# Kernel tuning notes

Measured on AMD Instinct MI355X. Metric: run time of the kernel, lower is better.

## Reference

```python
import math
import jax, jax.numpy as jnp
import numpy as np

D_MODEL = 1024
N_HEADS = 16
D_HEAD = D_MODEL // N_HEADS
MAX_REL = 1024
B = 2
S = 1024


def setup_inputs() -> dict:
    key = jax.random.key(0)
    ks = jax.random.split(key, 12)
    inp = {
        'query': jax.random.normal(ks[0], (B, S, D_MODEL), dtype=jnp.float32),
        'key': jax.random.normal(ks[1], (B, S, D_MODEL), dtype=jnp.float32),
        'value': jax.random.normal(ks[2], (B, S, D_MODEL), dtype=jnp.float32),
        # projection weights (torch nn.Linear: y = x @ W.T + b)
        'Wq': jax.random.normal(ks[3], (D_MODEL, D_MODEL), dtype=jnp.float32) / math.sqrt(D_MODEL),
        'bq': jax.random.normal(ks[4], (D_MODEL,), dtype=jnp.float32) * 0.02,
        'Wk': jax.random.normal(ks[5], (D_MODEL, D_MODEL), dtype=jnp.float32) / math.sqrt(D_MODEL),
        'bk': jax.random.normal(ks[6], (D_MODEL,), dtype=jnp.float32) * 0.02,
        'Wv': jax.random.normal(ks[7], (D_MODEL, D_MODEL), dtype=jnp.float32) / math.sqrt(D_MODEL),
        'bv': jax.random.normal(ks[8], (D_MODEL,), dtype=jnp.float32) * 0.02,
        # relative position tables (mask_future=True -> (max_rel, d_head))
        'rel_pos': jax.random.uniform(ks[9], (MAX_REL, D_HEAD), dtype=jnp.float32),
        'val_rel_pos': jax.random.uniform(ks[10], (MAX_REL, D_HEAD), dtype=jnp.float32),
    }
    return inp


def _rel_repr(table, seq_len):
    # mask_future=True branch: seq_len <= max_rel -> simple slice
    return table[:seq_len]  # [S, d_head]


def reference(query, key, value, Wq, bq, Wk, bk, Wv, bv, rel_pos, val_rel_pos):
    n_batch, seq_len, d_model = query.shape
    H, Dh = N_HEADS, D_HEAD

    def proj(x, W, b):
        return (x @ W.T + b).reshape(n_batch, seq_len, H, Dh).transpose(0, 2, 1, 3)

    q = proj(query, Wq, bq)   # [B,H,S,Dh]
    k = proj(key, Wk, bk)
    v = proj(value, Wv, bv)

    attn = jnp.einsum('bhid,bhjd->bhij', q, k)  # [B,H,S,S]

    # relative position bias via Music-Transformer skew trick (faithful to source)
    er = _rel_repr(rel_pos, seq_len)                 # [S, Dh]
    qe = jnp.einsum('bhid,rd->bhir', q, er)          # q @ er.T
    qe = jnp.flip(qe, axis=-1)
    qe = jnp.pad(qe, ((0, 0), (0, 0), (0, 0), (1, 0)))
    qe = qe.reshape(n_batch, H, seq_len + 1, seq_len)[:, :, 1:, :]
    attn = (attn + qe) / math.sqrt(Dh)               # source scales AFTER adding qe

    # causal future mask
    fmask = jnp.triu(jnp.ones((seq_len, seq_len), dtype=bool), k=1)
    attn = jnp.where(fmask[None, None], -jnp.inf, attn)
    attn = jax.nn.softmax(attn, axis=-1)

    z = jnp.einsum('bhij,bhjd->bhid', attn, v)

    # value relative position: zr[i] = sum_{j<=i} attn[i,j] * erv[i-j]
    # (equivalent to the source's flip/unfold construction of vr)
    erv = _rel_repr(val_rel_pos, seq_len)            # [S, Dh]
    i = jnp.arange(seq_len)[:, None]
    r = jnp.arange(seq_len)[None, :]
    j = i - r                                        # column index for relative dist r
    valid = (j >= 0).astype(attn.dtype)
    jc = jnp.clip(j, 0, seq_len - 1)
    attn_rel = jnp.take_along_axis(attn, jc[None, None], axis=-1) * valid[None, None]
    z = z + jnp.einsum('bhir,rd->bhid', attn_rel, erv)

    z = z.transpose(0, 2, 1, 3).reshape(n_batch, seq_len, d_model)
    return z
```

## Files before the change

kernel.cpp:

```cpp
#include <hip/hip_runtime.h>

typedef __bf16 bf16x8 __attribute__((ext_vector_type(8)));
typedef float f32x4 __attribute__((ext_vector_type(4)));

#define MFMA(a, b, c) __builtin_amdgcn_mfma_f32_16x16x32_bf16((a), (b), (c), 0, 0, 0)

#define DPPF(x, ctrl) __builtin_bit_cast(float, __builtin_amdgcn_mov_dpp(__builtin_bit_cast(int, (x)), (ctrl), 0xF, 0xF, true))

static __device__ __forceinline__ float rowmax16(float v) {
    v = fmaxf(v, DPPF(v, 0xB1));
    v = fmaxf(v, DPPF(v, 0x4E));
    v = fmaxf(v, DPPF(v, 0x124));
    v = fmaxf(v, DPPF(v, 0x128));
    return v;
}
static __device__ __forceinline__ float rowsum16(float v) {
    v += DPPF(v, 0xB1);
    v += DPPF(v, 0x4E);
    v += DPPF(v, 0x124);
    v += DPPF(v, 0x128);
    return v;
}

static __device__ __forceinline__ unsigned short f2b(float f) {
    unsigned int u = __builtin_bit_cast(unsigned int, f);
    unsigned int lsb = (u >> 16) & 1u;
    u += 0x7fffu + lsb;
    return (unsigned short)(u >> 16);
}

static __device__ __forceinline__ f32x4 zero4() {
    f32x4 z; z[0] = 0.f; z[1] = 0.f; z[2] = 0.f; z[3] = 0.f; return z;
}

typedef __attribute__((address_space(3))) unsigned int lds_as_t;
typedef const __attribute__((address_space(1))) unsigned int glb_as_t;
static __device__ __forceinline__ void gload16(const void* g, void* l) {
    __builtin_amdgcn_global_load_lds((glb_as_t*)g, (lds_as_t*)l, 16, 0, 0);
}

__global__ __launch_bounds__(256) void prep_convert(
    const float* __restrict__ q, const float* __restrict__ k, const float* __restrict__ v,
    const float* __restrict__ wq, const float* __restrict__ wk, const float* __restrict__ wv,
    const float* __restrict__ rel, const float* __restrict__ vrel,
    unsigned short* __restrict__ xq, unsigned short* __restrict__ xk, unsigned short* __restrict__ xv,
    unsigned short* __restrict__ wqb, unsigned short* __restrict__ wkb, unsigned short* __restrict__ wvb,
    unsigned short* __restrict__ erb, unsigned short* __restrict__ ervT)
{
    const int NG = 2375680;
    for (int g = blockIdx.x * 256 + threadIdx.x; g < NG + 69632; g += gridDim.x * 256) {
        if (g < NG) {
            const float* src; unsigned short* dst; int off;
            if (g < 1572864) {
                int s = g / 524288; off = g - s * 524288;
                src = s == 0 ? q : s == 1 ? k : v;
                dst = s == 0 ? xq : s == 1 ? xk : xv;
            } else if (g < 2359296) {
                int s = (g - 1572864) / 262144; off = g - 1572864 - s * 262144;
                src = s == 0 ? wq : s == 1 ? wk : wv;
                dst = s == 0 ? wqb : s == 1 ? wkb : wvb;
            } else {
                off = g - 2359296; src = rel; dst = erb;
            }
            float4 x = *(const float4*)(src + (size_t)off * 4);
            *(ushort4*)(dst + (size_t)off * 4) =
                make_ushort4(f2b(x.x), f2b(x.y), f2b(x.z), f2b(x.w));
        } else {
            int j = g - NG;
            int dh = j / 1088, c = j % 1088, r = c - 47;
            ervT[j] = (r >= 0 && r < 1024) ? f2b(vrel[r * 64 + dh]) : (unsigned short)0;
        }
    }
}

__global__ __launch_bounds__(256, 4) void proj_gemm2(
    const unsigned short* __restrict__ xq, const unsigned short* __restrict__ xk,
    const unsigned short* __restrict__ xv,
    const unsigned short* __restrict__ wqb, const unsigned short* __restrict__ wkb,
    const unsigned short* __restrict__ wvb,
    const float* __restrict__ bqp, const float* __restrict__ bkp, const float* __restrict__ bvp,
    unsigned short* __restrict__ oq, unsigned short* __restrict__ ok, unsigned short* __restrict__ ov)
{
    __shared__ unsigned short As[128][64];
    __shared__ unsigned short Bs[64][64];

    const int tid = threadIdx.x, lane = tid & 63, w = tid >> 6;
    const int bid = blockIdx.x;
    const int swz = (bid & 7) * 96 + (bid >> 3);
    const int mt = swz >> 4, nt = swz & 15;
    const int z = mt >> 4;
    const int mm0 = (mt & 15) * 128, n0 = nt * 64;

    const unsigned short* X = z == 0 ? xq : z == 1 ? xk : xv;
    const unsigned short* W = z == 0 ? wqb : z == 1 ? wkb : wvb;
    const float* bias = z == 0 ? bqp : z == 1 ? bkp : bvp;
    unsigned short* outp = z == 0 ? oq : z == 1 ? ok : ov;

    const int wm = (w & 1) * 64, wn = (w >> 1) * 32;
    const int lr = lane & 15, lg = lane >> 4;
    const int arow = lane >> 3, acol = (lane & 7) * 8;

    f32x4 acc[4][2];
#pragma unroll
    for (int a = 0; a < 4; ++a)
#pragma unroll
        for (int bq = 0; bq < 2; ++bq) acc[a][bq] = zero4();

    for (int k0 = 0; k0 < 1024; k0 += 64) {
#pragma unroll
        for (int c = 0; c < 4; ++c) {
            int ch = w + c * 4;
            gload16(X + (size_t)(mm0 + ch * 8 + arow) * 1024 + k0 + acol, &As[ch * 8][0]);
        }
#pragma unroll
        for (int c = 0; c < 2; ++c) {
            int ch = w + c * 4;
            gload16(W + (size_t)(n0 + ch * 8 + arow) * 1024 + k0 + acol, &Bs[ch * 8][0]);
        }
        __syncthreads();

        bf16x8 af[4][2], bg[2][2];
#pragma unroll
        for (int m4 = 0; m4 < 4; ++m4)
#pragma unroll
            for (int ks = 0; ks < 2; ++ks)
                af[m4][ks] = *(const bf16x8*)&As[wm + m4 * 16 + lr][ks * 32 + lg * 8];
#pragma unroll
        for (int n2 = 0; n2 < 2; ++n2)
#pragma unroll
            for (int ks = 0; ks < 2; ++ks)
                bg[n2][ks] = *(const bf16x8*)&Bs[wn + n2 * 16 + lr][ks * 32 + lg * 8];
#pragma unroll
        for (int m4 = 0; m4 < 4; ++m4)
#pragma unroll
            for (int n2 = 0; n2 < 2; ++n2)
#pragma unroll
                for (int ks = 0; ks < 2; ++ks)
                    acc[m4][n2] = MFMA(af[m4][ks], bg[n2][ks], acc[m4][n2]);
        __syncthreads();
    }

#pragma unroll
    for (int m4 = 0; m4 < 4; ++m4)
#pragma unroll
        for (int n2 = 0; n2 < 2; ++n2)
#pragma unroll
            for (int r = 0; r < 4; ++r) {
                int mrow = mm0 + wm + m4 * 16 + lg * 4 + r;
                int n = n0 + wn + n2 * 16 + lr;
                float vv = acc[m4][n2][r] + bias[n];
                if (z == 0) vv *= 0.125f;
                int b = mrow >> 10, s = mrow & 1023, h = n >> 6, dh = n & 63;
                unsigned short bv = f2b(vv);
                if (z == 2)
                    outp[(((size_t)(b * 16 + h)) * 64 + dh) * 1024 + s] = bv;
                else
                    outp[(((size_t)(b * 16 + h)) * 1024 + s) * 64 + dh] = bv;
            }
}

__global__ __launch_bounds__(256) void attn_kernel(
    const unsigned short* __restrict__ qb, const unsigned short* __restrict__ kb,
    const unsigned short* __restrict__ vtb, const unsigned short* __restrict__ erb,
    const unsigned short* __restrict__ ervT, float* __restrict__ out)
{
    const int bx = blockIdx.x, h = blockIdx.y, b = blockIdx.z;
    const int bh = b * 16 + h;
    const int tid = threadIdx.x;
    const int lane = tid & 63, w = tid >> 6;
    const int lr = lane & 15, lg = lane >> 4;

    __shared__ __align__(16) char smem[25600];
    float* qe_w = (float*)(smem + w * 3200);
    unsigned short* p_w   = (unsigned short*)(smem + 12800 + w * 1024);
    unsigned short* prv_w = (unsigned short*)(smem + 17408 + w * 2048);
    float* pO = (float*)smem;
    float* pm = (float*)(smem + 16896);
    float* pl = pm + 64;

    for (int t = lane; t < 16 * 64; t += 64) prv_w[t] = 0;

    for (int seg = 0; seg < 2; ++seg) {
        const int qt = seg == 0 ? bx : 63 - bx;
        const int i0 = qt * 16;

        const unsigned short* qbase = qb + (((size_t)bh * 1024) + i0 + lr) * 64 + lg * 8;
        const bf16x8 qf0 = *(const bf16x8*)qbase;
        const bf16x8 qf1 = *(const bf16x8*)(qbase + 32);

        f32x4 oacc[4];
        float m_run[4], l_run[4];
#pragma unroll
        for (int r = 0; r < 4; ++r) { oacc[r] = zero4(); m_run[r] = -1e30f; l_run[r] = 0.f; }

        const int ntiles = qt / 2 + 1;
        for (int ti = w; ti < ntiles; ti += 4) {
            const int j0 = ti * 32;
            const int dbp = i0 - j0 - 31;

            bf16x8 kf[2][2], ef[3][2], vf[4], rf[4][2];
#pragma unroll
            for (int ct = 0; ct < 2; ++ct) {
                const unsigned short* kbase =
                    kb + (((size_t)bh * 1024) + j0 + ct * 16 + lr) * 64 + lg * 8;
                kf[ct][0] = *(const bf16x8*)kbase;
                kf[ct][1] = *(const bf16x8*)(kbase + 32);
            }
#pragma unroll
            for (int st = 0; st < 3; ++st) {
                int dr = dbp + st * 16 + lr;
                dr = dr < 0 ? 0 : (dr > 1023 ? 1023 : dr);
                const unsigned short* eb = erb + (size_t)dr * 64 + lg * 8;
                ef[st][0] = *(const bf16x8*)eb;
                ef[st][1] = *(const bf16x8*)(eb + 32);
            }
#pragma unroll
            for (int dt = 0; dt < 4; ++dt)
                vf[dt] = *(const bf16x8*)(vtb + ((size_t)bh * 64 + dt * 16 + lr) * 1024 + j0 + lg * 8);
#pragma unroll
            for (int dt = 0; dt < 4; ++dt) {
                const unsigned short* rb2 =
                    ervT + (size_t)(dt * 16 + lr) * 1088 + 47 + dbp + lg * 8;
                rf[dt][0] = *(const bf16x8*)rb2;
                rf[dt][1] = *(const bf16x8*)(rb2 + 32);
            }

            f32x4 sacc[2]; sacc[0] = zero4(); sacc[1] = zero4();
#pragma unroll
            for (int ct = 0; ct < 2; ++ct) {
                sacc[ct] = MFMA(qf0, kf[ct][0], sacc[ct]);
                sacc[ct] = MFMA(qf1, kf[ct][1], sacc[ct]);
            }

            f32x4 qeacc[3];
#pragma unroll
            for (int st = 0; st < 3; ++st) {
                qeacc[st] = zero4();
                qeacc[st] = MFMA(qf0, ef[st][0], qeacc[st]);
                qeacc[st] = MFMA(qf1, ef[st][1], qeacc[st]);
            }

#pragma unroll
            for (int st = 0; st < 3; ++st)
#pragma unroll
                for (int r = 0; r < 4; ++r)
                    qe_w[(lg * 4 + r) * 50 + st * 16 + lr] = qeacc[st][r];

            float sc2[2][4];
#pragma unroll
            for (int ct = 0; ct < 2; ++ct)
#pragma unroll
                for (int r = 0; r < 4; ++r) {
                    int row  = lg * 4 + r;
                    int jcol = ct * 16 + lr;
                    int t    = row - jcol + 31;
                    float sc = sacc[ct][r] + qe_w[row * 50 + t];
                    if (j0 + jcol > i0 + row) sc = -1e38f;
                    sc2[ct][r] = sc;
                }

            float p2[2][4];
#pragma unroll
            for (int r = 0; r < 4; ++r) {
                float mx = rowmax16(fmaxf(sc2[0][r], sc2[1][r]));
                float mnew = fmaxf(m_run[r], mx);
                float scale = __expf(m_run[r] - mnew);
                float p0 = __expf(sc2[0][r] - mnew);
                float p1 = __expf(sc2[1][r] - mnew);
                float ps = rowsum16(p0 + p1);
                l_run[r] = l_run[r] * scale + ps;
                m_run[r] = mnew;
#pragma unroll
                for (int dt = 0; dt < 4; ++dt) oacc[dt][r] *= scale;
                p2[0][r] = p0; p2[1][r] = p1;
            }

#pragma unroll
            for (int ct = 0; ct < 2; ++ct)
#pragma unroll
                for (int r = 0; r < 4; ++r) {
                    int row = lg * 4 + r, col = ct * 16 + lr;
                    unsigned short pb = f2b(p2[ct][r]);
                    p_w[row * 32 + col] = pb;
                    prv_w[row * 64 + (row + 31 - col)] = pb;
                }

            bf16x8 pa   = *(const bf16x8*)&p_w[lr * 32 + lg * 8];
            bf16x8 pra0 = *(const bf16x8*)&prv_w[lr * 64 + lg * 8];
            bf16x8 pra1 = *(const bf16x8*)&prv_w[lr * 64 + 32 + lg * 8];
#pragma unroll
            for (int dt = 0; dt < 4; ++dt) {
                oacc[dt] = MFMA(pa, vf[dt], oacc[dt]);
                oacc[dt] = MFMA(pra0, rf[dt][0], oacc[dt]);
                oacc[dt] = MFMA(pra1, rf[dt][1], oacc[dt]);
            }
        }

        __syncthreads();
#pragma unroll
        for (int dt = 0; dt < 4; ++dt)
#pragma unroll
            for (int r = 0; r < 4; ++r)
                pO[w * 1024 + (lg * 4 + r) * 64 + dt * 16 + lr] = oacc[dt][r];
        if (lr == 0)
#pragma unroll
            for (int r = 0; r < 4; ++r) {
                pm[w * 16 + lg * 4 + r] = m_run[r];
                pl[w * 16 + lg * 4 + r] = l_run[r];
            }
        __syncthreads();

#pragma unroll
        for (int k = 0; k < 4; ++k) {
            int c = k * 256 + tid;
            int row = c >> 6, dh = c & 63;
            float m0 = pm[row], m1 = pm[16 + row], m2 = pm[32 + row], m3 = pm[48 + row];
            float mf = fmaxf(fmaxf(m0, m1), fmaxf(m2, m3));
            float e0 = __expf(m0 - mf), e1 = __expf(m1 - mf);
            float e2 = __expf(m2 - mf), e3 = __expf(m3 - mf);
            float den = e0 * pl[row] + e1 * pl[16 + row] + e2 * pl[32 + row] + e3 * pl[48 + row];
            float num = e0 * pO[row * 64 + dh]        + e1 * pO[1024 + row * 64 + dh]
                      + e2 * pO[2048 + row * 64 + dh] + e3 * pO[3072 + row * 64 + dh];
            out[((size_t)(b * 1024 + i0 + row)) * 1024 + h * 64 + dh] = num / den;
        }
        __syncthreads();
    }
}

extern "C" void kernel_launch(void* const* d_in, const int* in_sizes, int n_in,
                              void* d_out, int out_size, void* d_ws, size_t ws_size,
                              hipStream_t stream) {
    const float* query = (const float*)d_in[0];
    const float* key   = (const float*)d_in[1];
    const float* value = (const float*)d_in[2];
    const float* Wq    = (const float*)d_in[3];
    const float* bq    = (const float*)d_in[4];
    const float* Wk    = (const float*)d_in[5];
    const float* bk    = (const float*)d_in[6];
    const float* Wv    = (const float*)d_in[7];
    const float* bv    = (const float*)d_in[8];
    const float* rel   = (const float*)d_in[9];
    const float* vrel  = (const float*)d_in[10];
    float* out = (float*)d_out;

    char* w = (char*)d_ws;
    unsigned short* qb   = (unsigned short*)(w);
    unsigned short* kb   = (unsigned short*)(w + 4194304);
    unsigned short* vtb  = (unsigned short*)(w + 8388608);
    unsigned short* erb  = (unsigned short*)(w + 12582912);
    unsigned short* ervT = (unsigned short*)(w + 12713984);
    unsigned short* xq   = (unsigned short*)(w + 12853248);
    unsigned short* xk   = (unsigned short*)(w + 17047552);
    unsigned short* xv   = (unsigned short*)(w + 21241856);
    unsigned short* wqb  = (unsigned short*)(w + 25436160);
    unsigned short* wkb  = (unsigned short*)(w + 27533312);
    unsigned short* wvb  = (unsigned short*)(w + 29630464);

    prep_convert<<<dim3(2048), dim3(256), 0, stream>>>(
        query, key, value, Wq, Wk, Wv, rel, vrel,
        xq, xk, xv, wqb, wkb, wvb, erb, ervT);
    proj_gemm2<<<dim3(768), dim3(256), 0, stream>>>(
        xq, xk, xv, wqb, wkb, wvb, bq, bk, bv, qb, kb, vtb);
    attn_kernel<<<dim3(32, 16, 2), dim3(256), 0, stream>>>(qb, kb, vtb, erb, ervT, out);
}
```

Before: 217.0 us.

## Widen per-wave key tile to 64 columns to amortize softmax and relative-position overhead

```diff
diff --git a/kernel.cpp b/kernel.cpp
--- a/kernel.cpp
+++ b/kernel.cpp
@@ -159,7 +159,7 @@
             }
 }
 
-__global__ __launch_bounds__(256) void attn_kernel(
+__global__ __launch_bounds__(256, 1) void attn_kernel(
     const unsigned short* __restrict__ qb, const unsigned short* __restrict__ kb,
     const unsigned short* __restrict__ vtb, const unsigned short* __restrict__ erb,
     const unsigned short* __restrict__ ervT, float* __restrict__ out)
@@ -170,15 +170,15 @@
     const int lane = tid & 63, w = tid >> 6;
     const int lr = lane & 15, lg = lane >> 4;
 
-    __shared__ __align__(16) char smem[25600];
-    float* qe_w = (float*)(smem + w * 3200);
-    unsigned short* p_w   = (unsigned short*)(smem + 12800 + w * 1024);
-    unsigned short* prv_w = (unsigned short*)(smem + 17408 + w * 2048);
+    __shared__ __align__(16) char smem[41472];
+    float* qe_w = (float*)(smem + w * 5120);
+    unsigned short* p_w   = (unsigned short*)(smem + 20480 + w * 2048);
+    unsigned short* prv_w = (unsigned short*)(smem + 29184 + w * 3072);
     float* pO = (float*)smem;
-    float* pm = (float*)(smem + 16896);
+    float* pm = (float*)(smem + 28672);
     float* pl = pm + 64;
 
-    for (int t = lane; t < 16 * 64; t += 64) prv_w[t] = 0;
+    for (int t = lane; t < 16 * 96; t += 64) prv_w[t] = 0;
 
     for (int seg = 0; seg < 2; ++seg) {
         const int qt = seg == 0 ? bx : 63 - bx;
@@ -194,21 +194,22 @@
         for (int r = 0; r < 4; ++r) { oacc[r] = zero4(); m_run[r] = -1e30f; l_run[r] = 0.f; }
 
         const int ntiles = qt / 2 + 1;
-        for (int ti = w; ti < ntiles; ti += 4) {
-            const int j0 = ti * 32;
-            const int dbp = i0 - j0 - 31;
-
-            bf16x8 kf[2][2], ef[3][2], vf[4], rf[4][2];
-#pragma unroll
-            for (int ct = 0; ct < 2; ++ct) {
+        const int npairs = (ntiles + 1) >> 1;
+        for (int ti2 = w; ti2 < npairs; ti2 += 4) {
+            const int j0 = ti2 * 64;
+            const int dbp2 = i0 - j0 - 63;
+
+            bf16x8 kf[4][2], ef[5][2], vf[4][2], rf[4][3];
+#pragma unroll
+            for (int ct = 0; ct < 4; ++ct) {
                 const unsigned short* kbase =
                     kb + (((size_t)bh * 1024) + j0 + ct * 16 + lr) * 64 + lg * 8;
                 kf[ct][0] = *(const bf16x8*)kbase;
                 kf[ct][1] = *(const bf16x8*)(kbase + 32);
             }
 #pragma unroll
-            for (int st = 0; st < 3; ++st) {
-                int dr = dbp + st * 16 + lr;
+            for (int st = 0; st < 5; ++st) {
+                int dr = dbp2 + st * 16 + lr;
                 dr = dr < 0 ? 0 : (dr > 1023 ? 1023 : dr);
                 const unsigned short* eb = erb + (size_t)dr * 64 + lg * 8;
                 ef[st][0] = *(const bf16x8*)eb;
@@ -216,83 +217,93 @@
             }
 #pragma unroll
             for (int dt = 0; dt < 4; ++dt)
-                vf[dt] = *(const bf16x8*)(vtb + ((size_t)bh * 64 + dt * 16 + lr) * 1024 + j0 + lg * 8);
-#pragma unroll
-            for (int dt = 0; dt < 4; ++dt) {
-                const unsigned short* rb2 =
-                    ervT + (size_t)(dt * 16 + lr) * 1088 + 47 + dbp + lg * 8;
-                rf[dt][0] = *(const bf16x8*)rb2;
-                rf[dt][1] = *(const bf16x8*)(rb2 + 32);
-            }
-
-            f32x4 sacc[2]; sacc[0] = zero4(); sacc[1] = zero4();
-#pragma unroll
-            for (int ct = 0; ct < 2; ++ct) {
+#pragma unroll
+                for (int ks = 0; ks < 2; ++ks)
+                    vf[dt][ks] = *(const bf16x8*)(vtb + ((size_t)bh * 64 + dt * 16 + lr) * 1024
+                                                  + j0 + ks * 32 + lg * 8);
+#pragma unroll
+            for (int dt = 0; dt < 4; ++dt)
+#pragma unroll
+                for (int ks = 0; ks < 3; ++ks)
+                    rf[dt][ks] = *(const bf16x8*)(ervT + (size_t)(dt * 16 + lr) * 1088
+                                                  + 47 + dbp2 + ks * 32 + lg * 8);
+
+            f32x4 sacc[4];
+#pragma unroll
+            for (int ct = 0; ct < 4; ++ct) {
+                sacc[ct] = zero4();
                 sacc[ct] = MFMA(qf0, kf[ct][0], sacc[ct]);
                 sacc[ct] = MFMA(qf1, kf[ct][1], sacc[ct]);
             }
 
-            f32x4 qeacc[3];
-#pragma unroll
-            for (int st = 0; st < 3; ++st) {
+            f32x4 qeacc[5];
+#pragma unroll
+            for (int st = 0; st < 5; ++st) {
                 qeacc[st] = zero4();
                 qeacc[st] = MFMA(qf0, ef[st][0], qeacc[st]);
                 qeacc[st] = MFMA(qf1, ef[st][1], qeacc[st]);
             }
 
 #pragma unroll
-            for (int st = 0; st < 3; ++st)
+            for (int st = 0; st < 5; ++st)
 #pragma unroll
                 for (int r = 0; r < 4; ++r)
-                    qe_w[(lg * 4 + r) * 50 + st * 16 + lr] = qeacc[st][r];
-
-            float sc2[2][4];
-#pragma unroll
-            for (int ct = 0; ct < 2; ++ct)
+                    qe_w[(lg * 4 + r) * 80 + st * 16 + lr] = qeacc[st][r];
+
+            float sc2[4][4];
+#pragma unroll
+            for (int ct = 0; ct < 4; ++ct)
 #pragma unroll
                 for (int r = 0; r < 4; ++r) {
                     int row  = lg * 4 + r;
                     int jcol = ct * 16 + lr;
-                    int t    = row - jcol + 31;
-                    float sc = sacc[ct][r] + qe_w[row * 50 + t];
+                    int t    = row - jcol + 63;
+                    float sc = sacc[ct][r] + qe_w[row * 80 + t];
                     if (j0 + jcol > i0 + row) sc = -1e38f;
                     sc2[ct][r] = sc;
                 }
 
-            float p2[2][4];
+            float p2[4][4];
 #pragma unroll
             for (int r = 0; r < 4; ++r) {
-                float mx = rowmax16(fmaxf(sc2[0][r], sc2[1][r]));
+                float mx = fmaxf(fmaxf(sc2[0][r], sc2[1][r]), fmaxf(sc2[2][r], sc2[3][r]));
+                mx = rowmax16(mx);
                 float mnew = fmaxf(m_run[r], mx);
                 float scale = __expf(m_run[r] - mnew);
                 float p0 = __expf(sc2[0][r] - mnew);
                 float p1 = __expf(sc2[1][r] - mnew);
-                float ps = rowsum16(p0 + p1);
+                float p2_ = __expf(sc2[2][r] - mnew);
+                float p3 = __expf(sc2[3][r] - mnew);
+                float ps = rowsum16((p0 + p1) + (p2_ + p3));
                 l_run[r] = l_run[r] * scale + ps;
                 m_run[r] = mnew;
 #pragma unroll
                 for (int dt = 0; dt < 4; ++dt) oacc[dt][r] *= scale;
-                p2[0][r] = p0; p2[1][r] = p1;
-            }
-
-#pragma unroll
-            for (int ct = 0; ct < 2; ++ct)
+                p2[0][r] = p0; p2[1][r] = p1; p2[2][r] = p2_; p2[3][r] = p3;
+            }
+
+#pragma unroll
+            for (int ct = 0; ct < 4; ++ct)
 #pragma unroll
                 for (int r = 0; r < 4; ++r) {
                     int row = lg * 4 + r, col = ct * 16 + lr;
                     unsigned short pb = f2b(p2[ct][r]);
-                    p_w[row * 32 + col] = pb;
-                    prv_w[row * 64 + (row + 31 - col)] = pb;
+                    p_w[row * 64 + col] = pb;
+                    prv_w[row * 96 + (row + 63 - col)] = pb;
                 }
 
-            bf16x8 pa   = *(const bf16x8*)&p_w[lr * 32 + lg * 8];
-            bf16x8 pra0 = *(const bf16x8*)&prv_w[lr * 64 + lg * 8];
-            bf16x8 pra1 = *(const bf16x8*)&prv_w[lr * 64 + 32 + lg * 8];
+            bf16x8 pa0  = *(const bf16x8*)&p_w[lr * 64 + lg * 8];
+            bf16x8 pa1  = *(const bf16x8*)&p_w[lr * 64 + 32 + lg * 8];
+            bf16x8 pra0 = *(const bf16x8*)&prv_w[lr * 96 + lg * 8];
+            bf16x8 pra1 = *(const bf16x8*)&prv_w[lr * 96 + 32 + lg * 8];
+            bf16x8 pra2 = *(const bf16x8*)&prv_w[lr * 96 + 64 + lg * 8];
 #pragma unroll
             for (int dt = 0; dt < 4; ++dt) {
-                oacc[dt] = MFMA(pa, vf[dt], oacc[dt]);
+                oacc[dt] = MFMA(pa0, vf[dt][0], oacc[dt]);
+                oacc[dt] = MFMA(pa1, vf[dt][1], oacc[dt]);
                 oacc[dt] = MFMA(pra0, rf[dt][0], oacc[dt]);
                 oacc[dt] = MFMA(pra1, rf[dt][1], oacc[dt]);
+                oacc[dt] = MFMA(pra2, rf[dt][2], oacc[dt]);
             }
         }
 
```

New measurement: 204.4 us. 5.8% less time.
